# Optimization experiments

Measured on AMD Instinct MI355X. Metric: run time of the kernel, lower is better.

Reference implementation:

```python
import jax, jax.numpy as jnp
import numpy as np

MIDC = 128
HEADS = 8
HEADC = MIDC // HEADS
EPS = 1e-5


def setup_inputs() -> dict:
    key = jax.random.key(0)
    ks = jax.random.split(key, 7)
    B, C, H, W = 8, MIDC, 128, 128
    x = jax.random.normal(ks[0], (B, C, H, W), dtype=jnp.float32)
    s = 1.0 / np.sqrt(C)
    qkv_w = jax.random.normal(ks[1], (3 * C, C), dtype=jnp.float32) * s
    qkv_b = jnp.zeros((3 * C,), dtype=jnp.float32)
    o1_w = jax.random.normal(ks[2], (C, C), dtype=jnp.float32) * s
    o1_b = jnp.zeros((C,), dtype=jnp.float32)
    o2_w = jax.random.normal(ks[3], (C, C), dtype=jnp.float32) * s
    o2_b = jnp.zeros((C,), dtype=jnp.float32)
    kln_w = jnp.ones((HEADS, 1, HEADC), dtype=jnp.float32)
    kln_b = jnp.zeros((HEADS, 1, HEADC), dtype=jnp.float32)
    vln_w = jnp.ones((HEADS, 1, HEADC), dtype=jnp.float32)
    vln_b = jnp.zeros((HEADS, 1, HEADC), dtype=jnp.float32)
    return {"x": x, "qkv_w": qkv_w, "qkv_b": qkv_b, "o1_w": o1_w, "o1_b": o1_b,
            "o2_w": o2_w, "o2_b": o2_b, "kln_w": kln_w, "kln_b": kln_b,
            "vln_w": vln_w, "vln_b": vln_b}


def _layernorm(t, w, b):
    # torch LayerNorm clone: mean/std over last dim, std uses ddof=1 (unbiased)
    mean = t.mean(-1, keepdims=True)
    std = jnp.std(t, axis=-1, ddof=1, keepdims=True)
    return w * ((t - mean) / (std + EPS)) + b


def reference(x, qkv_w, qkv_b, o1_w, o1_b, o2_w, o2_b, kln_w, kln_b, vln_w, vln_b):
    B, C, H, W = x.shape
    N = H * W
    bias0 = x
    # 1x1 conv == pointwise linear over channels
    xf = x.transpose(0, 2, 3, 1).reshape(B, N, C)              # [B, N, C]
    qkv = xf @ qkv_w.T + qkv_b                                 # [B, N, 3C]
    qkv = qkv.reshape(B, N, HEADS, 3 * HEADC).transpose(0, 2, 1, 3)  # [B, h, N, 3d]
    q, k, v = jnp.split(qkv, 3, axis=-1)                       # each [B, h, N, d]
    k = _layernorm(k, kln_w, kln_b)
    v = _layernorm(v, vln_w, vln_b)
    kv = jnp.einsum('bhnd,bhne->bhde', k, v) / N               # [B, h, d, d]
    av = jnp.einsum('bhnd,bhde->bhne', q, kv)                  # [B, h, N, d]
    av = av.transpose(0, 2, 1, 3).reshape(B, H, W, C)
    ret = av.transpose(0, 3, 1, 2) + bias0                     # [B, C, H, W]
    # o_proj1 -> GELU -> o_proj2, residual
    rf = ret.transpose(0, 2, 3, 1)                             # [B, H, W, C]
    h1 = jax.nn.gelu(rf @ o1_w.T + o1_b, approximate=False)
    h2 = h1 @ o2_w.T + o2_b
    return h2.transpose(0, 3, 1, 2) + bias0
```

## Files before the change

### kernel.cpp

```cpp
#include <hip/hip_runtime.h>
#include <hip/hip_bf16.h>

#define LN_EPS 1e-5f

typedef __bf16 bf16x8 __attribute__((ext_vector_type(8)));
typedef float  f32x4  __attribute__((ext_vector_type(4)));
typedef unsigned short u16;
typedef unsigned int u32;

__device__ __forceinline__ u16 f2bf(float f) {
    __bf16 b = (__bf16)f;
    return __builtin_bit_cast(u16, b);
}
__device__ __forceinline__ bf16x8 zero8() {
    bf16x8 v;
#pragma unroll
    for (int j = 0; j < 8; j++) v[j] = (__bf16)0.f;
    return v;
}
__device__ __forceinline__ float gelu_f(float v) {
    float t = v * fmaf(v * v, 0.0713548162726f, 1.5957691216057f);
    return v / (1.f + __expf(-t));
}

__global__ __launch_bounds__(256) void prep_kernel(
    const float* __restrict__ qkv_w, const float* __restrict__ o1_w,
    const float* __restrict__ o2_w, u16* __restrict__ wq,
    u16* __restrict__ o1f, u16* __restrict__ o2f) {
    int i = blockIdx.x * 256 + threadIdx.x;
    if (i >= 81920) return;
    int j = i;
    const float* src;
    u16* dst;
    if (j < 49152) { src = qkv_w; dst = wq; }
    else if (j < 65536) { j -= 49152; src = o1_w; dst = o1f; }
    else { j -= 65536; src = o2_w; dst = o2f; }
    int jj = j & 7;
    int l  = (j >> 3) & 63;
    int s  = (j >> 9) & 3;
    int t  = j >> 11;
    int outc = t * 16 + (l & 15);
    int k    = s * 32 + ((l >> 4) & 3) * 8 + jj;
    dst[j] = f2bf(src[outc * 128 + k]);
}

__global__ __launch_bounds__(512, 6) void k1(
    const float* __restrict__ x, const u16* __restrict__ wq,
    const float* __restrict__ qkv_b,
    const float* __restrict__ klw, const float* __restrict__ klb,
    const float* __restrict__ vlw, const float* __restrict__ vlb,
    u16* __restrict__ q_ws, float* __restrict__ part) {
    __shared__ __align__(16) char Rbuf[51200];
    u16* x_a  = (u16*)Rbuf;
    u16* kv_s = (u16*)Rbuf;
    u16* q_s  = (u16*)(Rbuf + 33792);
    u16* kT   = (u16*)Rbuf;
    u16* vT   = (u16*)(Rbuf + 18432);

    const int tid  = threadIdx.x;
    const int lane = tid & 63;
    const int wv   = tid >> 6;
    const int stripe = wv >> 1;
    const int half   = wv & 1;
    const int bid  = blockIdx.x;
    const int b    = bid >> 8;
    const int n0   = (bid & 255) * 64;

    {
        int cw  = tid & 63;
        int sub = tid >> 6;
        const float* p0 = x + ((size_t)(b * 128 + 2 * cw)) * 16384 + n0 + sub * 8;
        const float* p1 = p0 + 16384;
        float4 a0 = ((const float4*)p0)[0], a1 = ((const float4*)p0)[1];
        float4 c0 = ((const float4*)p1)[0], c1 = ((const float4*)p1)[1];
        float av[8] = {a0.x, a0.y, a0.z, a0.w, a1.x, a1.y, a1.z, a1.w};
        float cv[8] = {c0.x, c0.y, c0.z, c0.w, c1.x, c1.y, c1.z, c1.w};
        u32* dst = (u32*)x_a;
#pragma unroll
        for (int j = 0; j < 8; j++)
            dst[(sub * 8 + j) * 68 + cw] = (u32)f2bf(av[j]) | ((u32)f2bf(cv[j]) << 16);
    }
    __syncthreads();

    const int m16  = stripe * 16;
    const int l15  = lane & 15;
    const int quad = lane >> 4;

    bf16x8 af[4];
#pragma unroll
    for (int s = 0; s < 4; s++)
        af[s] = *(const bf16x8*)&x_a[(m16 + l15) * 136 + s * 32 + quad * 8];
    __syncthreads();

    const int tb = half * 12;
#pragma unroll
    for (int hh = 0; hh < 4; hh++) {
        const int tq = tb + 3 * hh;
        f32x4 aq  = (f32x4){0.f, 0.f, 0.f, 0.f};
        f32x4 ak  = (f32x4){0.f, 0.f, 0.f, 0.f};
        f32x4 avv = (f32x4){0.f, 0.f, 0.f, 0.f};
#pragma unroll
        for (int s = 0; s < 4; s++) {
            bf16x8 bq = *(const bf16x8*)(wq + (size_t)(((tq + 0) * 4 + s) * 64 + lane) * 8);
            bf16x8 bk = *(const bf16x8*)(wq + (size_t)(((tq + 1) * 4 + s) * 64 + lane) * 8);
            bf16x8 bv = *(const bf16x8*)(wq + (size_t)(((tq + 2) * 4 + s) * 64 + lane) * 8);
            aq  = __builtin_amdgcn_mfma_f32_16x16x32_bf16(af[s], bq, aq, 0, 0, 0);
            ak  = __builtin_amdgcn_mfma_f32_16x16x32_bf16(af[s], bk, ak, 0, 0, 0);
            avv = __builtin_amdgcn_mfma_f32_16x16x32_bf16(af[s], bv, avv, 0, 0, 0);
        }
        const int h = half * 4 + hh;
        float biasq = qkv_b[(tq + 0) * 16 + l15];
        float biask = qkv_b[(tq + 1) * 16 + l15];
        float biasv = qkv_b[(tq + 2) * 16 + l15];
#pragma unroll
        for (int r = 0; r < 4; r++) {
            int row = m16 + quad * 4 + r;
            q_s[row * 136 + h * 16 + l15]       = f2bf(aq[r] + biasq);
            kv_s[row * 264 + h * 32 + l15]      = f2bf(ak[r] + biask);
            kv_s[row * 264 + h * 32 + 16 + l15] = f2bf(avv[r] + biasv);
        }
    }
    __syncthreads();

    {
#pragma unroll
        for (int p = 0; p < 2; p++) {
            int c = tid + p * 512;
            int lane_c = c & 63;
            int s  = (c >> 6) & 3;
            int tl = c >> 8;
            int row = tl * 16 + (lane_c & 15);
            const uint4* src = (const uint4*)&q_s[row * 136 + s * 32 + (lane_c >> 4) * 8];
            size_t gtile = (size_t)b * 1024 + (n0 >> 4) + tl;
            *(uint4*)(q_ws + gtile * 2048 + s * 512 + lane_c * 8) = *src;
        }
    }
    const int hL = __builtin_amdgcn_readfirstlane(wv);
    const u16* rowp = &kv_s[lane * 264 + hL * 32];
    bf16x8 rk0 = *(const bf16x8*)(rowp);
    bf16x8 rk1 = *(const bf16x8*)(rowp + 8);
    bf16x8 rv0 = *(const bf16x8*)(rowp + 16);
    bf16x8 rv1 = *(const bf16x8*)(rowp + 24);
    __syncthreads();

    {
        float kf[16], vf[16];
#pragma unroll
        for (int j = 0; j < 8; j++) {
            kf[j] = (float)rk0[j]; kf[8 + j] = (float)rk1[j];
            vf[j] = (float)rv0[j]; vf[8 + j] = (float)rv1[j];
        }
        float ksum = 0.f, ksq = 0.f, vsum = 0.f, vsq = 0.f;
#pragma unroll
        for (int d = 0; d < 16; d++) {
            ksum += kf[d]; ksq = fmaf(kf[d], kf[d], ksq);
            vsum += vf[d]; vsq = fmaf(vf[d], vf[d], vsq);
        }
        float km = ksum * (1.f / 16.f);
        float kvar = (ksq - 16.f * km * km) * (1.f / 15.f);
        kvar = kvar < 0.f ? 0.f : kvar;
        float kinv = 1.f / (sqrtf(kvar) + LN_EPS);
        float vm = vsum * (1.f / 16.f);
        float vvar = (vsq - 16.f * vm * vm) * (1.f / 15.f);
        vvar = vvar < 0.f ? 0.f : vvar;
        float vinv = 1.f / (sqrtf(vvar) + LN_EPS);
        const float* kwp = klw + hL * 16; const float* kbp = klb + hL * 16;
        const float* vwp = vlw + hL * 16; const float* vbp = vlb + hL * 16;
#pragma unroll
        for (int d = 0; d < 16; d++) {
            kT[(hL * 16 + d) * 72 + lane] = f2bf(fmaf((kf[d] - km) * kinv, kwp[d], kbp[d]));
            vT[(hL * 16 + d) * 72 + lane] = f2bf(fmaf((vf[d] - vm) * vinv, vwp[d], vbp[d]));
        }
    }
    __syncthreads();

    {
        const u16* ka = &kT[(hL * 16 + l15) * 72 + quad * 8];
        const u16* vb = &vT[(hL * 16 + l15) * 72 + quad * 8];
        bf16x8 A0 = *(const bf16x8*)(ka);
        bf16x8 A1 = *(const bf16x8*)(ka + 32);
        bf16x8 B0 = *(const bf16x8*)(vb);
        bf16x8 B1 = *(const bf16x8*)(vb + 32);
        f32x4 kv = __builtin_amdgcn_mfma_f32_16x16x32_bf16(A0, B0, (f32x4){0.f,0.f,0.f,0.f}, 0, 0, 0);
        kv = __builtin_amdgcn_mfma_f32_16x16x32_bf16(A1, B1, kv, 0, 0, 0);
        ((f32x4*)part)[(size_t)(bid * 8 + hL) * 64 + lane] = kv;
    }
}

__global__ __launch_bounds__(256) void k_red(const float* __restrict__ part,
                                             u16* __restrict__ kvf) {
    __shared__ float red[256];
    int tid = threadIdx.x;
    int b  = blockIdx.x >> 5;
    int eg = blockIdx.x & 31;
    int el = tid & 63;
    int tchunk = tid >> 6;
    int e = eg * 64 + el;
    int h = e >> 8, dk = (e >> 4) & 15, dv = e & 15;
    size_t off = (size_t)h * 256 + (size_t)(((dk >> 2) * 16 + dv) * 4 + (dk & 3));
    float s = 0.f;
#pragma unroll 8
    for (int t = tchunk * 64; t < tchunk * 64 + 64; t++)
        s += part[((size_t)(b * 256 + t)) * 2048 + off];
    red[tid] = s;
    __syncthreads();
    if (tid < 64) {
        float total = red[tid] + red[tid + 64] + red[tid + 128] + red[tid + 192];
        int e2 = eg * 64 + tid;
        int h2 = e2 >> 8, dk2 = (e2 >> 4) & 15, dv2 = e2 & 15;
        kvf[(size_t)(b * 8 + h2) * 256 + (dk2 >> 3) * 128 + dv2 * 8 + (dk2 & 7)] =
            f2bf(total * (1.f / 16384.f));
    }
}

__global__ __launch_bounds__(256, 5) void k2(
    const float* __restrict__ x, const u16* __restrict__ q_ws,
    const u16* __restrict__ kvf, const u16* __restrict__ o1f,
    const u16* __restrict__ o2f, const float* __restrict__ o1_b,
    const float* __restrict__ o2_b, float* __restrict__ out) {
    __shared__ u16 a_s[32 * 136];
    __shared__ float x_s[128 * 36];

    const int tid  = threadIdx.x;
    const int lane = tid & 63;
    const int wv   = tid >> 6;
    const int stripe = wv >> 1;
    const int half   = wv & 1;
    const int bid  = blockIdx.x;
    const int b    = bid >> 9;
    const int n0   = (bid & 511) * 32;

    const int m16  = stripe * 16;
    const int l15  = lane & 15;
    const int quad = lane >> 4;
    const bool act = quad < 2;

    bf16x8 qf[4], kvb[4];
    {
        size_t gtile = (size_t)b * 1024 + (n0 >> 4) + stripe;
#pragma unroll
        for (int hh = 0; hh < 4; hh++) {
            int h = half * 4 + hh;
            if (act) {
                int laneq = ((h & 1) * 2 + quad) * 16 + l15;
                qf[hh]  = *(const bf16x8*)(q_ws + gtile * 2048 + (h >> 1) * 512 + laneq * 8);
                kvb[hh] = *(const bf16x8*)(kvf + (size_t)(b * 8 + h) * 256 + quad * 128 + l15 * 8);
            } else {
                qf[hh] = zero8(); kvb[hh] = zero8();
            }
        }
    }

    {
        int c = tid >> 1, nh = (tid & 1) * 16;
        const float4* xs = (const float4*)(x + ((size_t)(b * 128 + c)) * 16384 + n0 + nh);
        float4* xd = (float4*)&x_s[c * 36 + nh];
#pragma unroll
        for (int i = 0; i < 4; i++) xd[i] = xs[i];
    }
    __syncthreads();

#pragma unroll
    for (int hh = 0; hh < 4; hh++) {
        int h = half * 4 + hh;
        f32x4 acc = __builtin_amdgcn_mfma_f32_16x16x32_bf16(
            qf[hh], kvb[hh], (f32x4){0.f,0.f,0.f,0.f}, 0, 0, 0);
#pragma unroll
        for (int r = 0; r < 4; r++) {
            float rv = acc[r] + x_s[(h * 16 + l15) * 36 + m16 + quad * 4 + r];
            a_s[(m16 + quad * 4 + r) * 136 + h * 16 + l15] = f2bf(rv);
        }
    }
    __syncthreads();

    bf16x8 af2[4];
#pragma unroll
    for (int s = 0; s < 4; s++)
        af2[s] = *(const bf16x8*)&a_s[(m16 + l15) * 136 + s * 32 + quad * 8];
    f32x4 acc2[4];
#pragma unroll
    for (int t = 0; t < 4; t++) acc2[t] = (f32x4){0.f,0.f,0.f,0.f};
#pragma unroll
    for (int tt = 0; tt < 4; tt++) {
        int t = half * 4 + tt;
#pragma unroll
        for (int s = 0; s < 4; s++) {
            bf16x8 bf = *(const bf16x8*)(o1f + (size_t)((t * 4 + s) * 64 + lane) * 8);
            acc2[tt] = __builtin_amdgcn_mfma_f32_16x16x32_bf16(af2[s], bf, acc2[tt], 0, 0, 0);
        }
    }
    float g[4][4];
#pragma unroll
    for (int tt = 0; tt < 4; tt++) {
        float bb = o1_b[(half * 4 + tt) * 16 + l15];
#pragma unroll
        for (int r = 0; r < 4; r++)
            g[tt][r] = gelu_f(acc2[tt][r] + bb);
    }
    __syncthreads();
#pragma unroll
    for (int tt = 0; tt < 4; tt++)
#pragma unroll
        for (int r = 0; r < 4; r++)
            a_s[(m16 + quad * 4 + r) * 136 + (half * 4 + tt) * 16 + l15] = f2bf(g[tt][r]);
    __syncthreads();

#pragma unroll
    for (int s = 0; s < 4; s++)
        af2[s] = *(const bf16x8*)&a_s[(m16 + l15) * 136 + s * 32 + quad * 8];
#pragma unroll
    for (int t = 0; t < 4; t++) acc2[t] = (f32x4){0.f,0.f,0.f,0.f};
#pragma unroll
    for (int tt = 0; tt < 4; tt++) {
        int t = half * 4 + tt;
#pragma unroll
        for (int s = 0; s < 4; s++) {
            bf16x8 bf = *(const bf16x8*)(o2f + (size_t)((t * 4 + s) * 64 + lane) * 8);
            acc2[tt] = __builtin_amdgcn_mfma_f32_16x16x32_bf16(af2[s], bf, acc2[tt], 0, 0, 0);
        }
    }
#pragma unroll
    for (int tt = 0; tt < 4; tt++) {
        int t = half * 4 + tt;
        float bb = o2_b[t * 16 + l15];
#pragma unroll
        for (int r = 0; r < 4; r++) {
            int row = m16 + quad * 4 + r;
            int col = t * 16 + l15;
            x_s[col * 36 + row] = acc2[tt][r] + bb + x_s[col * 36 + row];
        }
    }
    __syncthreads();

    {
        int c = tid >> 1, nh = (tid & 1) * 16;
        float4* dst = (float4*)(out + ((size_t)(b * 128 + c)) * 16384 + n0 + nh);
        const float4* sv = (const float4*)&x_s[c * 36 + nh];
#pragma unroll
        for (int i = 0; i < 4; i++) dst[i] = sv[i];
    }
}

extern "C" void kernel_launch(void* const* d_in, const int* in_sizes, int n_in,
                              void* d_out, int out_size, void* d_ws, size_t ws_size,
                              hipStream_t stream) {
    (void)in_sizes; (void)n_in; (void)out_size; (void)ws_size;
    const float* x     = (const float*)d_in[0];
    const float* qkv_w = (const float*)d_in[1];
    const float* qkv_b = (const float*)d_in[2];
    const float* o1_w  = (const float*)d_in[3];
    const float* o1_b  = (const float*)d_in[4];
    const float* o2_w  = (const float*)d_in[5];
    const float* o2_b  = (const float*)d_in[6];
    const float* klw   = (const float*)d_in[7];
    const float* klb   = (const float*)d_in[8];
    const float* vlw   = (const float*)d_in[9];
    const float* vlb   = (const float*)d_in[10];
    float* outp = (float*)d_out;

    char* ws = (char*)d_ws;
    u16*   kvf  = (u16*)(ws);
    u16*   wq   = (u16*)(ws + 32768);
    u16*   o1f  = (u16*)(ws + 131072);
    u16*   o2f  = (u16*)(ws + 163840);
    float* part = (float*)(ws + 196608);
    u16*   q_ws = (u16*)(ws + 196608 + 16777216);

    prep_kernel<<<320, 256, 0, stream>>>(qkv_w, o1_w, o2_w, wq, o1f, o2f);
    k1<<<2048, 512, 0, stream>>>(x, wq, qkv_b, klw, klb, vlw, vlb, q_ws, part);
    k_red<<<256, 256, 0, stream>>>(part, kvf);
    k2<<<4096, 256, 0, stream>>>(x, q_ws, kvf, o1f, o2f, o1_b, o2_b, outp);
}
```

Before: 206.0 us.

## Shrink k1 to 256-thread blocks looping over two 32-row subtiles

Measured after the change: 564.6 us. 2.74x slower.

```diff
diff --git a/kernel.cpp b/kernel.cpp
--- a/kernel.cpp
+++ b/kernel.cpp
@@ -44,18 +44,18 @@
     dst[j] = f2bf(src[outc * 128 + k]);
 }
 
-__global__ __launch_bounds__(512, 6) void k1(
+__global__ __launch_bounds__(256, 6) void k1(
     const float* __restrict__ x, const u16* __restrict__ wq,
     const float* __restrict__ qkv_b,
     const float* __restrict__ klw, const float* __restrict__ klb,
     const float* __restrict__ vlw, const float* __restrict__ vlb,
     u16* __restrict__ q_ws, float* __restrict__ part) {
-    __shared__ __align__(16) char Rbuf[51200];
+    __shared__ __align__(16) char Rbuf[25600];
     u16* x_a  = (u16*)Rbuf;
     u16* kv_s = (u16*)Rbuf;
-    u16* q_s  = (u16*)(Rbuf + 33792);
+    u16* q_s  = (u16*)(Rbuf + 16896);
     u16* kT   = (u16*)Rbuf;
-    u16* vT   = (u16*)(Rbuf + 18432);
+    u16* vT   = (u16*)(Rbuf + 10240);
 
     const int tid  = threadIdx.x;
     const int lane = tid & 63;
@@ -64,126 +64,140 @@
     const int half   = wv & 1;
     const int bid  = blockIdx.x;
     const int b    = bid >> 8;
-    const int n0   = (bid & 255) * 64;
-
-    {
-        int cw  = tid & 63;
-        int sub = tid >> 6;
-        const float* p0 = x + ((size_t)(b * 128 + 2 * cw)) * 16384 + n0 + sub * 8;
-        const float* p1 = p0 + 16384;
-        float4 a0 = ((const float4*)p0)[0], a1 = ((const float4*)p0)[1];
-        float4 c0 = ((const float4*)p1)[0], c1 = ((const float4*)p1)[1];
-        float av[8] = {a0.x, a0.y, a0.z, a0.w, a1.x, a1.y, a1.z, a1.w};
-        float cv[8] = {c0.x, c0.y, c0.z, c0.w, c1.x, c1.y, c1.z, c1.w};
-        u32* dst = (u32*)x_a;
-#pragma unroll
-        for (int j = 0; j < 8; j++)
-            dst[(sub * 8 + j) * 68 + cw] = (u32)f2bf(av[j]) | ((u32)f2bf(cv[j]) << 16);
-    }
-    __syncthreads();
+    const int tile0 = (bid & 255) * 64;
 
     const int m16  = stripe * 16;
     const int l15  = lane & 15;
     const int quad = lane >> 4;
-
-    bf16x8 af[4];
-#pragma unroll
-    for (int s = 0; s < 4; s++)
-        af[s] = *(const bf16x8*)&x_a[(m16 + l15) * 136 + s * 32 + quad * 8];
-    __syncthreads();
-
-    const int tb = half * 12;
-#pragma unroll
-    for (int hh = 0; hh < 4; hh++) {
-        const int tq = tb + 3 * hh;
-        f32x4 aq  = (f32x4){0.f, 0.f, 0.f, 0.f};
-        f32x4 ak  = (f32x4){0.f, 0.f, 0.f, 0.f};
-        f32x4 avv = (f32x4){0.f, 0.f, 0.f, 0.f};
-#pragma unroll
-        for (int s = 0; s < 4; s++) {
-            bf16x8 bq = *(const bf16x8*)(wq + (size_t)(((tq + 0) * 4 + s) * 64 + lane) * 8);
-            bf16x8 bk = *(const bf16x8*)(wq + (size_t)(((tq + 1) * 4 + s) * 64 + lane) * 8);
-            bf16x8 bv = *(const bf16x8*)(wq + (size_t)(((tq + 2) * 4 + s) * 64 + lane) * 8);
-            aq  = __builtin_amdgcn_mfma_f32_16x16x32_bf16(af[s], bq, aq, 0, 0, 0);
-            ak  = __builtin_amdgcn_mfma_f32_16x16x32_bf16(af[s], bk, ak, 0, 0, 0);
-            avv = __builtin_amdgcn_mfma_f32_16x16x32_bf16(af[s], bv, avv, 0, 0, 0);
-        }
-        const int h = half * 4 + hh;
-        float biasq = qkv_b[(tq + 0) * 16 + l15];
-        float biask = qkv_b[(tq + 1) * 16 + l15];
-        float biasv = qkv_b[(tq + 2) * 16 + l15];
-#pragma unroll
-        for (int r = 0; r < 4; r++) {
-            int row = m16 + quad * 4 + r;
-            q_s[row * 136 + h * 16 + l15]       = f2bf(aq[r] + biasq);
-            kv_s[row * 264 + h * 32 + l15]      = f2bf(ak[r] + biask);
-            kv_s[row * 264 + h * 32 + 16 + l15] = f2bf(avv[r] + biasv);
-        }
-    }
-    __syncthreads();
-
-    {
-#pragma unroll
-        for (int p = 0; p < 2; p++) {
-            int c = tid + p * 512;
-            int lane_c = c & 63;
-            int s  = (c >> 6) & 3;
-            int tl = c >> 8;
-            int row = tl * 16 + (lane_c & 15);
-            const uint4* src = (const uint4*)&q_s[row * 136 + s * 32 + (lane_c >> 4) * 8];
-            size_t gtile = (size_t)b * 1024 + (n0 >> 4) + tl;
-            *(uint4*)(q_ws + gtile * 2048 + s * 512 + lane_c * 8) = *src;
-        }
-    }
-    const int hL = __builtin_amdgcn_readfirstlane(wv);
-    const u16* rowp = &kv_s[lane * 264 + hL * 32];
-    bf16x8 rk0 = *(const bf16x8*)(rowp);
-    bf16x8 rk1 = *(const bf16x8*)(rowp + 8);
-    bf16x8 rv0 = *(const bf16x8*)(rowp + 16);
-    bf16x8 rv1 = *(const bf16x8*)(rowp + 24);
-    __syncthreads();
-
-    {
-        float kf[16], vf[16];
-#pragma unroll
-        for (int j = 0; j < 8; j++) {
-            kf[j] = (float)rk0[j]; kf[8 + j] = (float)rk1[j];
-            vf[j] = (float)rv0[j]; vf[8 + j] = (float)rv1[j];
-        }
-        float ksum = 0.f, ksq = 0.f, vsum = 0.f, vsq = 0.f;
-#pragma unroll
-        for (int d = 0; d < 16; d++) {
-            ksum += kf[d]; ksq = fmaf(kf[d], kf[d], ksq);
-            vsum += vf[d]; vsq = fmaf(vf[d], vf[d], vsq);
-        }
-        float km = ksum * (1.f / 16.f);
-        float kvar = (ksq - 16.f * km * km) * (1.f / 15.f);
-        kvar = kvar < 0.f ? 0.f : kvar;
-        float kinv = 1.f / (sqrtf(kvar) + LN_EPS);
-        float vm = vsum * (1.f / 16.f);
-        float vvar = (vsq - 16.f * vm * vm) * (1.f / 15.f);
-        vvar = vvar < 0.f ? 0.f : vvar;
-        float vinv = 1.f / (sqrtf(vvar) + LN_EPS);
-        const float* kwp = klw + hL * 16; const float* kbp = klb + hL * 16;
-        const float* vwp = vlw + hL * 16; const float* vbp = vlb + hL * 16;
-#pragma unroll
-        for (int d = 0; d < 16; d++) {
-            kT[(hL * 16 + d) * 72 + lane] = f2bf(fmaf((kf[d] - km) * kinv, kwp[d], kbp[d]));
-            vT[(hL * 16 + d) * 72 + lane] = f2bf(fmaf((vf[d] - vm) * vinv, vwp[d], vbp[d]));
-        }
-    }
-    __syncthreads();
-
-    {
-        const u16* ka = &kT[(hL * 16 + l15) * 72 + quad * 8];
-        const u16* vb = &vT[(hL * 16 + l15) * 72 + quad * 8];
-        bf16x8 A0 = *(const bf16x8*)(ka);
-        bf16x8 A1 = *(const bf16x8*)(ka + 32);
-        bf16x8 B0 = *(const bf16x8*)(vb);
-        bf16x8 B1 = *(const bf16x8*)(vb + 32);
-        f32x4 kv = __builtin_amdgcn_mfma_f32_16x16x32_bf16(A0, B0, (f32x4){0.f,0.f,0.f,0.f}, 0, 0, 0);
-        kv = __builtin_amdgcn_mfma_f32_16x16x32_bf16(A1, B1, kv, 0, 0, 0);
-        ((f32x4*)part)[(size_t)(bid * 8 + hL) * 64 + lane] = kv;
+    const int hL   = wv * 2 + (lane >> 5);
+    const int rown = lane & 31;
+
+    f32x4 kvacc[2];
+#pragma unroll
+    for (int hh = 0; hh < 2; hh++) kvacc[hh] = (f32x4){0.f, 0.f, 0.f, 0.f};
+
+    for (int it = 0; it < 2; ++it) {
+        if (it) __syncthreads();
+        const int n0 = tile0 + it * 32;
+
+        {
+            int cw  = tid & 63;
+            int sub = tid >> 6;
+            const float* p0 = x + ((size_t)(b * 128 + 2 * cw)) * 16384 + n0 + sub * 8;
+            const float* p1 = p0 + 16384;
+            float4 a0 = ((const float4*)p0)[0], a1 = ((const float4*)p0)[1];
+            float4 c0 = ((const float4*)p1)[0], c1 = ((const float4*)p1)[1];
+            float av[8] = {a0.x, a0.y, a0.z, a0.w, a1.x, a1.y, a1.z, a1.w};
+            float cv[8] = {c0.x, c0.y, c0.z, c0.w, c1.x, c1.y, c1.z, c1.w};
+            u32* dst = (u32*)x_a;
+#pragma unroll
+            for (int j = 0; j < 8; j++)
+                dst[(sub * 8 + j) * 68 + cw] = (u32)f2bf(av[j]) | ((u32)f2bf(cv[j]) << 16);
+        }
+        __syncthreads();
+
+        bf16x8 af[4];
+#pragma unroll
+        for (int s = 0; s < 4; s++)
+            af[s] = *(const bf16x8*)&x_a[(m16 + l15) * 136 + s * 32 + quad * 8];
+        __syncthreads();
+
+        const int tb = half * 12;
+#pragma unroll
+        for (int hh = 0; hh < 4; hh++) {
+            const int tq = tb + 3 * hh;
+            f32x4 aq  = (f32x4){0.f, 0.f, 0.f, 0.f};
+            f32x4 ak  = (f32x4){0.f, 0.f, 0.f, 0.f};
+            f32x4 avv = (f32x4){0.f, 0.f, 0.f, 0.f};
+#pragma unroll
+            for (int s = 0; s < 4; s++) {
+                bf16x8 bq = *(const bf16x8*)(wq + (size_t)(((tq + 0) * 4 + s) * 64 + lane) * 8);
+                bf16x8 bk = *(const bf16x8*)(wq + (size_t)(((tq + 1) * 4 + s) * 64 + lane) * 8);
+                bf16x8 bv = *(const bf16x8*)(wq + (size_t)(((tq + 2) * 4 + s) * 64 + lane) * 8);
+                aq  = __builtin_amdgcn_mfma_f32_16x16x32_bf16(af[s], bq, aq, 0, 0, 0);
+                ak  = __builtin_amdgcn_mfma_f32_16x16x32_bf16(af[s], bk, ak, 0, 0, 0);
+                avv = __builtin_amdgcn_mfma_f32_16x16x32_bf16(af[s], bv, avv, 0, 0, 0);
+            }
+            const int h = half * 4 + hh;
+            float biasq = qkv_b[(tq + 0) * 16 + l15];
+            float biask = qkv_b[(tq + 1) * 16 + l15];
+            float biasv = qkv_b[(tq + 2) * 16 + l15];
+#pragma unroll
+            for (int r = 0; r < 4; r++) {
+                int row = m16 + quad * 4 + r;
+                q_s[row * 136 + h * 16 + l15]       = f2bf(aq[r] + biasq);
+                kv_s[row * 264 + h * 32 + l15]      = f2bf(ak[r] + biask);
+                kv_s[row * 264 + h * 32 + 16 + l15] = f2bf(avv[r] + biasv);
+            }
+        }
+        __syncthreads();
+
+        {
+#pragma unroll
+            for (int p = 0; p < 2; p++) {
+                int c = tid + p * 256;
+                int lane_c = c & 63;
+                int s  = (c >> 6) & 3;
+                int tl = c >> 8;
+                int row = tl * 16 + (lane_c & 15);
+                const uint4* src = (const uint4*)&q_s[row * 136 + s * 32 + (lane_c >> 4) * 8];
+                size_t gtile = (size_t)b * 1024 + (n0 >> 4) + tl;
+                *(uint4*)(q_ws + gtile * 2048 + s * 512 + lane_c * 8) = *src;
+            }
+        }
+        const u16* rowp = &kv_s[rown * 264 + hL * 32];
+        bf16x8 rk0 = *(const bf16x8*)(rowp);
+        bf16x8 rk1 = *(const bf16x8*)(rowp + 8);
+        bf16x8 rv0 = *(const bf16x8*)(rowp + 16);
+        bf16x8 rv1 = *(const bf16x8*)(rowp + 24);
+        __syncthreads();
+
+        {
+            float kf[16], vf[16];
+#pragma unroll
+            for (int j = 0; j < 8; j++) {
+                kf[j] = (float)rk0[j]; kf[8 + j] = (float)rk1[j];
+                vf[j] = (float)rv0[j]; vf[8 + j] = (float)rv1[j];
+            }
+            float ksum = 0.f, ksq = 0.f, vsum = 0.f, vsq = 0.f;
+#pragma unroll
+            for (int d = 0; d < 16; d++) {
+                ksum += kf[d]; ksq = fmaf(kf[d], kf[d], ksq);
+                vsum += vf[d]; vsq = fmaf(vf[d], vf[d], vsq);
+            }
+            float km = ksum * (1.f / 16.f);
+            float kvar = (ksq - 16.f * km * km) * (1.f / 15.f);
+            kvar = kvar < 0.f ? 0.f : kvar;
+            float kinv = 1.f / (sqrtf(kvar) + LN_EPS);
+            float vm = vsum * (1.f / 16.f);
+            float vvar = (vsq - 16.f * vm * vm) * (1.f / 15.f);
+            vvar = vvar < 0.f ? 0.f : vvar;
+            float vinv = 1.f / (sqrtf(vvar) + LN_EPS);
+            const float* kwp = klw + hL * 16; const float* kbp = klb + hL * 16;
+            const float* vwp = vlw + hL * 16; const float* vbp = vlb + hL * 16;
+#pragma unroll
+            for (int d = 0; d < 16; d++) {
+                kT[(hL * 16 + d) * 40 + rown] = f2bf(fmaf((kf[d] - km) * kinv, kwp[d], kbp[d]));
+                vT[(hL * 16 + d) * 40 + rown] = f2bf(fmaf((vf[d] - vm) * vinv, vwp[d], vbp[d]));
+            }
+        }
+        __syncthreads();
+
+#pragma unroll
+        for (int hh = 0; hh < 2; hh++) {
+            const int h = wv * 2 + hh;
+            const u16* ka = &kT[(h * 16 + l15) * 40 + quad * 8];
+            const u16* vb = &vT[(h * 16 + l15) * 40 + quad * 8];
+            bf16x8 A0 = *(const bf16x8*)(ka);
+            bf16x8 B0 = *(const bf16x8*)(vb);
+            kvacc[hh] = __builtin_amdgcn_mfma_f32_16x16x32_bf16(A0, B0, kvacc[hh], 0, 0, 0);
+        }
+    }
+
+#pragma unroll
+    for (int hh = 0; hh < 2; hh++) {
+        const int h = wv * 2 + hh;
+        ((f32x4*)part)[(size_t)(bid * 8 + h) * 64 + lane] = kvacc[hh];
     }
 }
 
@@ -367,7 +381,7 @@
     u16*   q_ws = (u16*)(ws + 196608 + 16777216);
 
     prep_kernel<<<320, 256, 0, stream>>>(qkv_w, o1_w, o2_w, wq, o1f, o2f);
-    k1<<<2048, 512, 0, stream>>>(x, wq, qkv_b, klw, klb, vlw, vlb, q_ws, part);
+    k1<<<2048, 256, 0, stream>>>(x, wq, qkv_b, klw, klb, vlw, vlb, q_ws, part);
     k_red<<<256, 256, 0, stream>>>(part, kvf);
     k2<<<4096, 256, 0, stream>>>(x, q_ws, kvf, o1f, o2f, o1_b, o2_b, outp);
 }
```
